# Kernel tuning notes

Measured on AMD Instinct MI355X. Metric: run time of the kernel, lower is better.

## Reference

```python
import jax, jax.numpy as jnp
import numpy as np

B, T, E, U, V = 4096, 80, 100, 64, 10000

def setup_inputs() -> dict:
    key = jax.random.key(0)
    ks = jax.random.split(key, 10)
    s = lambda *sh: 0.05
    return {
        "tokens": jax.random.randint(ks[0], (B, T), 0, V, dtype=jnp.int32),
        "emb": jax.random.normal(ks[1], (V, E), jnp.float32) * 0.05,
        "k0": jax.random.normal(ks[2], (E, 4 * U), jnp.float32) * 0.05,
        "r0": jax.random.normal(ks[3], (U, 4 * U), jnp.float32) * 0.05,
        "b0": jnp.zeros((4 * U,), jnp.float32),
        "k1": jax.random.normal(ks[4], (E, 4 * U), jnp.float32) * 0.05,
        "r1": jax.random.normal(ks[5], (U, 4 * U), jnp.float32) * 0.05,
        "b1": jnp.zeros((4 * U,), jnp.float32),
        "Wd": jax.random.normal(ks[6], (U, 1), jnp.float32) * 0.05,
        "bd": jnp.zeros((1,), jnp.float32),
    }

def _lstm_cell(h, c, xt, k, r, b):
    # keras LSTMCell gate order: i, f, g(cell candidate), o
    z = xt @ k + h @ r + b  # [B, 4U]
    i, f, g, o = jnp.split(z, 4, axis=-1)
    c_new = jax.nn.sigmoid(f) * c + jax.nn.sigmoid(i) * jnp.tanh(g)
    h_new = jax.nn.sigmoid(o) * jnp.tanh(c_new)
    return h_new, c_new

def reference(tokens, emb, k0, r0, b0, k1, r1, b1, Wd, bd):
    x = emb[tokens]                 # [B, T, E]
    xs = jnp.swapaxes(x, 0, 1)      # [T, B, E] for scan over time
    zeros = jnp.zeros((tokens.shape[0], U), x.dtype)
    init = (zeros, zeros, zeros, zeros)  # h0, c0, h1, c1

    def step(state, xt):
        h0, c0, h1, c1 = state
        h0, c0 = _lstm_cell(h0, c0, xt, k0, r0, b0)
        # NOTE: original feeds the raw embedded word (not out0) to cell 1
        h1, c1 = _lstm_cell(h1, c1, xt, k1, r1, b1)
        return (h0, c0, h1, c1), None

    (h0, c0, h1, c1), _ = jax.lax.scan(step, init, xs)
    logits = h1 @ Wd + bd           # [B, 1]
    return jax.nn.sigmoid(logits)
```

## Files before the change

kernel.cpp:

```cpp
#include <hip/hip_runtime.h>
#include <hip/hip_bf16.h>

#define B_  4096
#define T_  80
#define E_  100
#define U_  64
#define G_  256
#define V_  10000

#define S_H  72
#define AS   136

typedef __attribute__((ext_vector_type(8))) __bf16 bf16x8;
typedef __attribute__((ext_vector_type(4))) __bf16 bf16x4;
typedef __attribute__((ext_vector_type(4))) float  floatx4;

__device__ __forceinline__ float sigmoidf_(float x) {
    return __builtin_amdgcn_rcpf(1.f + __expf(-x));
}

__device__ __forceinline__ float tanhf_(float x) {
    return fmaf(-2.f, __builtin_amdgcn_rcpf(__expf(2.f * x) + 1.f), 1.f);
}

__device__ __forceinline__ void block_sync_lgkm() {
    asm volatile("s_waitcnt lgkmcnt(0)\n\ts_barrier" ::: "memory");
}

__global__ __launch_bounds__(256) void embk_kernel(const float* __restrict__ emb,
                                                   const float* __restrict__ k1,
                                                   const float* __restrict__ b1,
                                                   float* __restrict__ embk) {
    __shared__ __bf16 aLDS[64 * AS];

    const int tid  = threadIdx.x;
    const int lane = tid & 63;
    const int w    = tid >> 6;
    const int n    = lane & 15;
    const int kg   = lane >> 4;
    const int v0   = (blockIdx.x >> 1) * 64;
    const int n0   = (blockIdx.x & 1) * 128;
    const int nrows = min(64, V_ - v0);

    for (int i = tid; i < 64 * AS / 8; i += 256) {
        bf16x8 z;
#pragma unroll
        for (int jj = 0; jj < 8; ++jj) z[jj] = (__bf16)0.f;
        *(bf16x8*)(aLDS + i * 8) = z;
    }

    bf16x8 bfr[2][4];
#pragma unroll
    for (int ct = 0; ct < 2; ++ct)
#pragma unroll
        for (int kc = 0; kc < 4; ++kc) {
            bf16x8 s;
#pragma unroll
            for (int jj = 0; jj < 8; ++jj) {
                int k = kc * 32 + kg * 8 + jj;
                s[jj] = (k < E_) ? (__bf16)k1[k * G_ + n0 + w * 32 + ct * 16 + n]
                                 : (__bf16)0.f;
            }
            bfr[ct][kc] = s;
        }
    const float bv0 = b1[n0 + w * 32 + n];
    const float bv1 = b1[n0 + w * 32 + 16 + n];

    __syncthreads();

    for (int i = tid; i < nrows * 25; i += 256) {
        int r = i / 25, q = i - r * 25;
        float4 ev = *(const float4*)(emb + (long)(v0 + r) * E_ + q * 4);
        bf16x4 bv; bv[0] = (__bf16)ev.x; bv[1] = (__bf16)ev.y;
                   bv[2] = (__bf16)ev.z; bv[3] = (__bf16)ev.w;
        *(bf16x4*)(aLDS + r * AS + q * 4) = bv;
    }
    __syncthreads();

#pragma unroll
    for (int mt = 0; mt < 4; ++mt) {
        const __bf16* ab = aLDS + (mt * 16 + n) * AS + kg * 8;
        bf16x8 a0 = *(const bf16x8*)(ab + 0);
        bf16x8 a1 = *(const bf16x8*)(ab + 32);
        bf16x8 a2 = *(const bf16x8*)(ab + 64);
        bf16x8 a3 = *(const bf16x8*)(ab + 96);
#pragma unroll
        for (int ct = 0; ct < 2; ++ct) {
            float bv = ct ? bv1 : bv0;
            floatx4 acc = {bv, bv, bv, bv};
            acc = __builtin_amdgcn_mfma_f32_16x16x32_bf16(a0, bfr[ct][0], acc, 0, 0, 0);
            acc = __builtin_amdgcn_mfma_f32_16x16x32_bf16(a1, bfr[ct][1], acc, 0, 0, 0);
            acc = __builtin_amdgcn_mfma_f32_16x16x32_bf16(a2, bfr[ct][2], acc, 0, 0, 0);
            acc = __builtin_amdgcn_mfma_f32_16x16x32_bf16(a3, bfr[ct][3], acc, 0, 0, 0);
#pragma unroll
            for (int r = 0; r < 4; ++r) {
                int v = v0 + mt * 16 + kg * 4 + r;
                if (v < V_) embk[(long)v * G_ + n0 + w * 32 + ct * 16 + n] = acc[r];
            }
        }
    }
}

__global__ __launch_bounds__(256) void lstm_kernel(const int*   __restrict__ tokens,
                                                   const float* __restrict__ embk,
                                                   const float* __restrict__ r1,
                                                   const float* __restrict__ Wd,
                                                   const float* __restrict__ bd,
                                                   float* __restrict__ out) {
    __shared__ int    tokLDS[16 * T_];
    __shared__ __bf16 hbuf[2][16 * S_H];

    const int tid  = threadIdx.x;
    const int lane = tid & 63;
    const int w    = tid >> 6;
    const int n    = lane & 15;
    const int kg   = lane >> 4;
    const int bb   = blockIdx.x * 16;

    for (int i = tid; i < 16 * T_; i += 256) tokLDS[i] = tokens[bb * T_ + i];
    for (int i = tid; i < 2 * 16 * S_H; i += 256) (&hbuf[0][0])[i] = (__bf16)0.f;

    bf16x8 afr[4][2];
#pragma unroll
    for (int ct = 0; ct < 4; ++ct)
#pragma unroll
        for (int kc = 0; kc < 2; ++kc) {
            bf16x8 s;
#pragma unroll
            for (int jj = 0; jj < 8; ++jj)
                s[jj] = (__bf16)r1[(kc * 32 + kg * 8 + jj) * G_ + ct * 64 + w * 16 + n];
            afr[ct][kc] = s;
        }

    float c[4] = {0.f, 0.f, 0.f, 0.f};

    __syncthreads();

    floatx4 xkb[2][4];
#pragma unroll
    for (int s = 0; s < 2; ++s) {
        const float* base = embk + (long)tokLDS[n * T_ + s] * G_ + w * 16 + kg * 4;
#pragma unroll
        for (int ct = 0; ct < 4; ++ct)
            xkb[s][ct] = *(const floatx4*)(base + ct * 64);
    }

    auto step = [&](int t, int sel) {
        const __bf16* hb = hbuf[sel ^ 1];
        bf16x8 b0 = *(const bf16x8*)(hb + n * S_H + kg * 8);
        bf16x8 b1 = *(const bf16x8*)(hb + n * S_H + 32 + kg * 8);

        floatx4 acc[4];
#pragma unroll
        for (int ct = 0; ct < 4; ++ct) {
            floatx4 a = xkb[sel][ct];
            a = __builtin_amdgcn_mfma_f32_16x16x32_bf16(afr[ct][0], b0, a, 0, 0, 0);
            a = __builtin_amdgcn_mfma_f32_16x16x32_bf16(afr[ct][1], b1, a, 0, 0, 0);
            acc[ct] = a;
        }

        if (t + 2 < T_) {
            const float* base = embk + (long)tokLDS[n * T_ + t + 2] * G_ + w * 16 + kg * 4;
#pragma unroll
            for (int ct = 0; ct < 4; ++ct)
                xkb[sel][ct] = *(const floatx4*)(base + ct * 64);
        }

        bf16x4 hv;
#pragma unroll
        for (int r = 0; r < 4; ++r) {
            float zi = acc[0][r], zf = acc[1][r], zg = acc[2][r], zo = acc[3][r];
            float cn = fmaf(sigmoidf_(zf), c[r], sigmoidf_(zi) * tanhf_(zg));
            float hn = sigmoidf_(zo) * tanhf_(cn);
            c[r] = cn;
            hv[r] = (__bf16)hn;
        }
        *(bf16x4*)(&hbuf[sel][0] + n * S_H + w * 16 + kg * 4) = hv;

        block_sync_lgkm();
    };

    for (int t = 0; t < T_; t += 2) {
        step(t,     0);
        step(t + 1, 1);
    }

    if (tid < 16) {
        const __bf16* hb = hbuf[1] + tid * S_H;
        float s = bd[0];
#pragma unroll
        for (int u = 0; u < U_; ++u) s = fmaf((float)hb[u], Wd[u], s);
        out[bb + tid] = sigmoidf_(s);
    }
}

extern "C" void kernel_launch(void* const* d_in, const int* in_sizes, int n_in,
                              void* d_out, int out_size, void* d_ws, size_t ws_size,
                              hipStream_t stream) {
    const int*   tokens = (const int*)  d_in[0];
    const float* emb    = (const float*)d_in[1];
    const float* k1     = (const float*)d_in[5];
    const float* r1     = (const float*)d_in[6];
    const float* b1     = (const float*)d_in[7];
    const float* Wd     = (const float*)d_in[8];
    const float* bd     = (const float*)d_in[9];
    float*       out    = (float*)d_out;

    float* embk = (float*)d_ws;

    embk_kernel<<<((V_ + 63) / 64) * 2, 256, 0, stream>>>(emb, k1, b1, embk);
    lstm_kernel<<<B_ / 16, 256, 0, stream>>>(tokens, embk, r1, Wd, bd, out);
}
```

Before: 145.0 us.

## Fuse embedding-input projection into LSTM kernel with pipelined per-step MFMA

Drops the separate kernel that precomputed a V×4U table of embedding times k1 plus bias. The LSTM kernel now loads raw embedding rows for upcoming tokens and computes the input projection with extra MFMAs inside each step, using a two-stage prefetch (load for t+2, build for t+1). This removes one kernel launch and the 10 MB table write and read, at the cost of four times more MFMA work per step and higher register pressure from the k1 fragments. Launch bounds are set to one block per SM and the token LDS rows are padded to avoid bank conflicts.

```diff
diff --git a/kernel.cpp b/kernel.cpp
--- a/kernel.cpp
+++ b/kernel.cpp
@@ -9,7 +9,7 @@
 #define V_  10000
 
 #define S_H  72
-#define AS   136
+#define TS   81
 
 typedef __attribute__((ext_vector_type(8))) __bf16 bf16x8;
 typedef __attribute__((ext_vector_type(4))) __bf16 bf16x4;
@@ -27,87 +27,22 @@
     asm volatile("s_waitcnt lgkmcnt(0)\n\ts_barrier" ::: "memory");
 }
 
-__global__ __launch_bounds__(256) void embk_kernel(const float* __restrict__ emb,
-                                                   const float* __restrict__ k1,
-                                                   const float* __restrict__ b1,
-                                                   float* __restrict__ embk) {
-    __shared__ __bf16 aLDS[64 * AS];
-
-    const int tid  = threadIdx.x;
-    const int lane = tid & 63;
-    const int w    = tid >> 6;
-    const int n    = lane & 15;
-    const int kg   = lane >> 4;
-    const int v0   = (blockIdx.x >> 1) * 64;
-    const int n0   = (blockIdx.x & 1) * 128;
-    const int nrows = min(64, V_ - v0);
-
-    for (int i = tid; i < 64 * AS / 8; i += 256) {
-        bf16x8 z;
-#pragma unroll
-        for (int jj = 0; jj < 8; ++jj) z[jj] = (__bf16)0.f;
-        *(bf16x8*)(aLDS + i * 8) = z;
-    }
-
-    bf16x8 bfr[2][4];
-#pragma unroll
-    for (int ct = 0; ct < 2; ++ct)
-#pragma unroll
-        for (int kc = 0; kc < 4; ++kc) {
-            bf16x8 s;
-#pragma unroll
-            for (int jj = 0; jj < 8; ++jj) {
-                int k = kc * 32 + kg * 8 + jj;
-                s[jj] = (k < E_) ? (__bf16)k1[k * G_ + n0 + w * 32 + ct * 16 + n]
-                                 : (__bf16)0.f;
-            }
-            bfr[ct][kc] = s;
-        }
-    const float bv0 = b1[n0 + w * 32 + n];
-    const float bv1 = b1[n0 + w * 32 + 16 + n];
-
-    __syncthreads();
-
-    for (int i = tid; i < nrows * 25; i += 256) {
-        int r = i / 25, q = i - r * 25;
-        float4 ev = *(const float4*)(emb + (long)(v0 + r) * E_ + q * 4);
-        bf16x4 bv; bv[0] = (__bf16)ev.x; bv[1] = (__bf16)ev.y;
-                   bv[2] = (__bf16)ev.z; bv[3] = (__bf16)ev.w;
-        *(bf16x4*)(aLDS + r * AS + q * 4) = bv;
-    }
-    __syncthreads();
-
-#pragma unroll
-    for (int mt = 0; mt < 4; ++mt) {
-        const __bf16* ab = aLDS + (mt * 16 + n) * AS + kg * 8;
-        bf16x8 a0 = *(const bf16x8*)(ab + 0);
-        bf16x8 a1 = *(const bf16x8*)(ab + 32);
-        bf16x8 a2 = *(const bf16x8*)(ab + 64);
-        bf16x8 a3 = *(const bf16x8*)(ab + 96);
-#pragma unroll
-        for (int ct = 0; ct < 2; ++ct) {
-            float bv = ct ? bv1 : bv0;
-            floatx4 acc = {bv, bv, bv, bv};
-            acc = __builtin_amdgcn_mfma_f32_16x16x32_bf16(a0, bfr[ct][0], acc, 0, 0, 0);
-            acc = __builtin_amdgcn_mfma_f32_16x16x32_bf16(a1, bfr[ct][1], acc, 0, 0, 0);
-            acc = __builtin_amdgcn_mfma_f32_16x16x32_bf16(a2, bfr[ct][2], acc, 0, 0, 0);
-            acc = __builtin_amdgcn_mfma_f32_16x16x32_bf16(a3, bfr[ct][3], acc, 0, 0, 0);
-#pragma unroll
-            for (int r = 0; r < 4; ++r) {
-                int v = v0 + mt * 16 + kg * 4 + r;
-                if (v < V_) embk[(long)v * G_ + n0 + w * 32 + ct * 16 + n] = acc[r];
-            }
-        }
-    }
-}
-
-__global__ __launch_bounds__(256) void lstm_kernel(const int*   __restrict__ tokens,
-                                                   const float* __restrict__ embk,
-                                                   const float* __restrict__ r1,
-                                                   const float* __restrict__ Wd,
-                                                   const float* __restrict__ bd,
-                                                   float* __restrict__ out) {
-    __shared__ int    tokLDS[16 * T_];
+__device__ __forceinline__ bf16x8 cvt8(const float4& a, const float4& b) {
+    bf16x8 r;
+    r[0] = (__bf16)a.x; r[1] = (__bf16)a.y; r[2] = (__bf16)a.z; r[3] = (__bf16)a.w;
+    r[4] = (__bf16)b.x; r[5] = (__bf16)b.y; r[6] = (__bf16)b.z; r[7] = (__bf16)b.w;
+    return r;
+}
+
+__global__ __launch_bounds__(256, 1) void lstm_kernel(const int*   __restrict__ tokens,
+                                                      const float* __restrict__ emb,
+                                                      const float* __restrict__ k1,
+                                                      const float* __restrict__ r1,
+                                                      const float* __restrict__ b1,
+                                                      const float* __restrict__ Wd,
+                                                      const float* __restrict__ bd,
+                                                      float* __restrict__ out) {
+    __shared__ int    tokLDS[16 * TS];
     __shared__ __bf16 hbuf[2][16 * S_H];
 
     const int tid  = threadIdx.x;
@@ -117,7 +52,8 @@
     const int kg   = lane >> 4;
     const int bb   = blockIdx.x * 16;
 
-    for (int i = tid; i < 16 * T_; i += 256) tokLDS[i] = tokens[bb * T_ + i];
+    for (int i = tid; i < 16 * T_; i += 256)
+        tokLDS[(i / T_) * TS + (i % T_)] = tokens[bb * T_ + i];
     for (int i = tid; i < 2 * 16 * S_H; i += 256) (&hbuf[0][0])[i] = (__bf16)0.f;
 
     bf16x8 afr[4][2];
@@ -132,38 +68,92 @@
             afr[ct][kc] = s;
         }
 
+    bf16x8 kfr[4][4];
+#pragma unroll
+    for (int ct = 0; ct < 4; ++ct)
+#pragma unroll
+        for (int kc = 0; kc < 4; ++kc) {
+            bf16x8 s;
+#pragma unroll
+            for (int jj = 0; jj < 8; ++jj) {
+                int k = kc * 32 + kg * 8 + jj;
+                s[jj] = (k < E_) ? (__bf16)k1[k * G_ + ct * 64 + w * 16 + n]
+                                 : (__bf16)0.f;
+            }
+            kfr[ct][kc] = s;
+        }
+
+    floatx4 bias[4];
+#pragma unroll
+    for (int ct = 0; ct < 4; ++ct)
+#pragma unroll
+        for (int r = 0; r < 4; ++r)
+            bias[ct][r] = b1[ct * 64 + w * 16 + kg * 4 + r];
+
     float c[4] = {0.f, 0.f, 0.f, 0.f};
 
     __syncthreads();
 
-    floatx4 xkb[2][4];
-#pragma unroll
-    for (int s = 0; s < 2; ++s) {
-        const float* base = embk + (long)tokLDS[n * T_ + s] * G_ + w * 16 + kg * 4;
-#pragma unroll
-        for (int ct = 0; ct < 4; ++ct)
-            xkb[s][ct] = *(const floatx4*)(base + ct * 64);
-    }
-
-    auto step = [&](int t, int sel) {
-        const __bf16* hb = hbuf[sel ^ 1];
-        bf16x8 b0 = *(const bf16x8*)(hb + n * S_H + kg * 8);
-        bf16x8 b1 = *(const bf16x8*)(hb + n * S_H + 32 + kg * 8);
+    const int trow = n * TS;
+
+    auto ldstage = [&](int tk, float4* st) {
+        const float* base = emb + (long)tk * E_;
+#pragma unroll
+        for (int kc = 0; kc < 3; ++kc) {
+            st[kc * 2]     = *(const float4*)(base + kc * 32 + kg * 8);
+            st[kc * 2 + 1] = *(const float4*)(base + kc * 32 + kg * 8 + 4);
+        }
+        st[6] = *(const float4*)(base + 96);
+    };
+
+    auto xbuild = [&](const float4* st, floatx4* xo) {
+        bf16x8 x0 = cvt8(st[0], st[1]);
+        bf16x8 x1 = cvt8(st[2], st[3]);
+        bf16x8 x2 = cvt8(st[4], st[5]);
+        float4 e3 = st[6];
+        if (kg) { e3.x = 0.f; e3.y = 0.f; e3.z = 0.f; e3.w = 0.f; }
+        bf16x8 x3;
+        x3[0] = (__bf16)e3.x; x3[1] = (__bf16)e3.y;
+        x3[2] = (__bf16)e3.z; x3[3] = (__bf16)e3.w;
+        x3[4] = (__bf16)0.f;  x3[5] = (__bf16)0.f;
+        x3[6] = (__bf16)0.f;  x3[7] = (__bf16)0.f;
+#pragma unroll
+        for (int ct = 0; ct < 4; ++ct) {
+            floatx4 a = bias[ct];
+            a = __builtin_amdgcn_mfma_f32_16x16x32_bf16(kfr[ct][0], x0, a, 0, 0, 0);
+            a = __builtin_amdgcn_mfma_f32_16x16x32_bf16(kfr[ct][1], x1, a, 0, 0, 0);
+            a = __builtin_amdgcn_mfma_f32_16x16x32_bf16(kfr[ct][2], x2, a, 0, 0, 0);
+            a = __builtin_amdgcn_mfma_f32_16x16x32_bf16(kfr[ct][3], x3, a, 0, 0, 0);
+            xo[ct] = a;
+        }
+    };
+
+    float4  stA[7], stB[7];
+    floatx4 xaccA[4], xaccB[4];
+
+    ldstage(tokLDS[trow + 0], stA);
+    xbuild(stA, xaccA);
+    ldstage(tokLDS[trow + 1], stB);
+    int tkA = tokLDS[trow + 2];
+    int tkB = tokLDS[trow + 3];
+
+    auto step = [&](int t, const __bf16* hbR, __bf16* hbW,
+                    floatx4* xuse, floatx4* xbld,
+                    float4* stuse, float4* stbld, int& tkpf) {
+        bf16x8 b0  = *(const bf16x8*)(hbR + n * S_H + kg * 8);
+        bf16x8 b1v = *(const bf16x8*)(hbR + n * S_H + 32 + kg * 8);
+
+        ldstage(tkpf, stbld);
+        int tnext = t + 4; if (tnext > T_ - 1) tnext = T_ - 1;
+        tkpf = tokLDS[trow + tnext];
 
         floatx4 acc[4];
 #pragma unroll
         for (int ct = 0; ct < 4; ++ct) {
-            floatx4 a = xkb[sel][ct];
-            a = __builtin_amdgcn_mfma_f32_16x16x32_bf16(afr[ct][0], b0, a, 0, 0, 0);
-            a = __builtin_amdgcn_mfma_f32_16x16x32_bf16(afr[ct][1], b1, a, 0, 0, 0);
+            floatx4 a = xuse[ct];
+            a = __builtin_amdgcn_mfma_f32_16x16x32_bf16(afr[ct][0], b0,  a, 0, 0, 0);
+            a = __builtin_amdgcn_mfma_f32_16x16x32_bf16(afr[ct][1], b1v, a, 0, 0, 0);
             acc[ct] = a;
-        }
-
-        if (t + 2 < T_) {
-            const float* base = embk + (long)tokLDS[n * T_ + t + 2] * G_ + w * 16 + kg * 4;
-#pragma unroll
-            for (int ct = 0; ct < 4; ++ct)
-                xkb[sel][ct] = *(const floatx4*)(base + ct * 64);
         }
 
         bf16x4 hv;
@@ -175,14 +165,16 @@
             c[r] = cn;
             hv[r] = (__bf16)hn;
         }
-        *(bf16x4*)(&hbuf[sel][0] + n * S_H + w * 16 + kg * 4) = hv;
+        *(bf16x4*)(hbW + n * S_H + w * 16 + kg * 4) = hv;
+
+        xbuild(stuse, xbld);
 
         block_sync_lgkm();
     };
 
     for (int t = 0; t < T_; t += 2) {
-        step(t,     0);
-        step(t + 1, 1);
+        step(t,     hbuf[1], hbuf[0], xaccA, xaccB, stB, stA, tkA);
+        step(t + 1, hbuf[0], hbuf[1], xaccB, xaccA, stA, stB, tkB);
     }
 
     if (tid < 16) {
@@ -206,8 +198,5 @@
     const float* bd     = (const float*)d_in[9];
     float*       out    = (float*)d_out;
 
-    float* embk = (float*)d_ws;
-
-    embk_kernel<<<((V_ + 63) / 64) * 2, 256, 0, stream>>>(emb, k1, b1, embk);
-    lstm_kernel<<<B_ / 16, 256, 0, stream>>>(tokens, embk, r1, Wd, bd, out);
-}
+    lstm_kernel<<<B_ / 16, 256, 0, stream>>>(tokens, emb, k1, r1, b1, Wd, bd, out);
+}
```

New measurement: 154.2 us. 1.06x slower.

## Stage gathered embedding projections through LDS ring buffer with coalesced prefetch

Applied to the files above, without the earlier changes.

The LSTM kernel now gathers the per-token precomputed input projections with coalesced float4 loads (16 threads per row) into registers, writes them into a three-slot LDS ring, and reads them back in the MFMA accumulator layout. Before, each lane did scattered gathers straight into accumulator registers. The gather is issued three steps ahead to hide global latency behind the recurrence. The embk kernel also stages k1 through LDS with coalesced loads instead of strided scalar loads. The cost is extra LDS traffic and more shared memory per block, which may reduce occupancy.

```diff
diff --git a/kernel.cpp b/kernel.cpp
--- a/kernel.cpp
+++ b/kernel.cpp
@@ -10,6 +10,9 @@
 
 #define S_H  72
 #define AS   136
+#define KS2  132
+#define TS   81
+#define XS   260
 
 typedef __attribute__((ext_vector_type(8))) __bf16 bf16x8;
 typedef __attribute__((ext_vector_type(4))) __bf16 bf16x4;
@@ -32,6 +35,7 @@
                                                    const float* __restrict__ b1,
                                                    float* __restrict__ embk) {
     __shared__ __bf16 aLDS[64 * AS];
+    __shared__ __bf16 kLDS[128 * KS2];
 
     const int tid  = threadIdx.x;
     const int lane = tid & 63;
@@ -48,21 +52,9 @@
         for (int jj = 0; jj < 8; ++jj) z[jj] = (__bf16)0.f;
         *(bf16x8*)(aLDS + i * 8) = z;
     }
-
-    bf16x8 bfr[2][4];
-#pragma unroll
-    for (int ct = 0; ct < 2; ++ct)
-#pragma unroll
-        for (int kc = 0; kc < 4; ++kc) {
-            bf16x8 s;
-#pragma unroll
-            for (int jj = 0; jj < 8; ++jj) {
-                int k = kc * 32 + kg * 8 + jj;
-                s[jj] = (k < E_) ? (__bf16)k1[k * G_ + n0 + w * 32 + ct * 16 + n]
-                                 : (__bf16)0.f;
-            }
-            bfr[ct][kc] = s;
-        }
+    for (int i = tid; i < 28 * KS2; i += 256)
+        kLDS[100 * KS2 + i] = (__bf16)0.f;
+
     const float bv0 = b1[n0 + w * 32 + n];
     const float bv1 = b1[n0 + w * 32 + 16 + n];
 
@@ -75,7 +67,26 @@
                    bv[2] = (__bf16)ev.z; bv[3] = (__bf16)ev.w;
         *(bf16x4*)(aLDS + r * AS + q * 4) = bv;
     }
+    for (int i = tid; i < 100 * 32; i += 256) {
+        int k = i >> 5, cq = (i & 31) * 4;
+        float4 kv = *(const float4*)(k1 + (long)k * G_ + n0 + cq);
+        bf16x4 bv; bv[0] = (__bf16)kv.x; bv[1] = (__bf16)kv.y;
+                   bv[2] = (__bf16)kv.z; bv[3] = (__bf16)kv.w;
+        *(bf16x4*)(kLDS + k * KS2 + cq) = bv;
+    }
     __syncthreads();
+
+    bf16x8 bfr[2][4];
+#pragma unroll
+    for (int ct = 0; ct < 2; ++ct)
+#pragma unroll
+        for (int kc = 0; kc < 4; ++kc) {
+            bf16x8 s;
+#pragma unroll
+            for (int jj = 0; jj < 8; ++jj)
+                s[jj] = kLDS[(kc * 32 + kg * 8 + jj) * KS2 + w * 32 + ct * 16 + n];
+            bfr[ct][kc] = s;
+        }
 
 #pragma unroll
     for (int mt = 0; mt < 4; ++mt) {
@@ -107,8 +118,9 @@
                                                    const float* __restrict__ Wd,
                                                    const float* __restrict__ bd,
                                                    float* __restrict__ out) {
-    __shared__ int    tokLDS[16 * T_];
+    __shared__ int    tokLDS[16 * TS];
     __shared__ __bf16 hbuf[2][16 * S_H];
+    __shared__ float  xstage[3][16 * XS];
 
     const int tid  = threadIdx.x;
     const int lane = tid & 63;
@@ -116,8 +128,11 @@
     const int n    = lane & 15;
     const int kg   = lane >> 4;
     const int bb   = blockIdx.x * 16;
-
-    for (int i = tid; i < 16 * T_; i += 256) tokLDS[i] = tokens[bb * T_ + i];
+    const int prow = tid >> 4;
+    const int pp   = tid & 15;
+
+    for (int i = tid; i < 16 * T_; i += 256)
+        tokLDS[(i / T_) * TS + (i % T_)] = tokens[bb * T_ + i];
     for (int i = tid; i < 2 * 16 * S_H; i += 256) (&hbuf[0][0])[i] = (__bf16)0.f;
 
     bf16x8 afr[4][2];
@@ -136,34 +151,54 @@
 
     __syncthreads();
 
-    floatx4 xkb[2][4];
-#pragma unroll
-    for (int s = 0; s < 2; ++s) {
-        const float* base = embk + (long)tokLDS[n * T_ + s] * G_ + w * 16 + kg * 4;
-#pragma unroll
-        for (int ct = 0; ct < 4; ++ct)
-            xkb[s][ct] = *(const floatx4*)(base + ct * 64);
-    }
-
-    auto step = [&](int t, int sel) {
+    float4 pf[2][4];
+    {
+#pragma unroll
+        for (int s = 0; s < 2; ++s) {
+            const float* base = embk + (long)tokLDS[prow * TS + s] * G_ + pp * 4;
+            float* dst = xstage[s] + prow * XS + pp * 4;
+#pragma unroll
+            for (int j = 0; j < 4; ++j)
+                *(float4*)(dst + j * 64) = *(const float4*)(base + j * 64);
+        }
+        const float* base2 = embk + (long)tokLDS[prow * TS + 2] * G_ + pp * 4;
+#pragma unroll
+        for (int j = 0; j < 4; ++j)
+            pf[1][j] = *(const float4*)(base2 + j * 64);
+    }
+    block_sync_lgkm();
+
+    auto step = [&](int t, int sel, int rb, int wb) {
         const __bf16* hb = hbuf[sel ^ 1];
-        bf16x8 b0 = *(const bf16x8*)(hb + n * S_H + kg * 8);
-        bf16x8 b1 = *(const bf16x8*)(hb + n * S_H + 32 + kg * 8);
+        bf16x8 b0  = *(const bf16x8*)(hb + n * S_H + kg * 8);
+        bf16x8 b1v = *(const bf16x8*)(hb + n * S_H + 32 + kg * 8);
+        const float* xrow = xstage[rb] + n * XS + w * 16 + kg * 4;
+        floatx4 x0 = *(const floatx4*)(xrow + 0);
+        floatx4 x1 = *(const floatx4*)(xrow + 64);
+        floatx4 x2 = *(const floatx4*)(xrow + 128);
+        floatx4 x3 = *(const floatx4*)(xrow + 192);
+
+        {
+            float* dst = xstage[wb] + prow * XS + pp * 4;
+            *(float4*)(dst +   0) = pf[sel ^ 1][0];
+            *(float4*)(dst +  64) = pf[sel ^ 1][1];
+            *(float4*)(dst + 128) = pf[sel ^ 1][2];
+            *(float4*)(dst + 192) = pf[sel ^ 1][3];
+        }
+        {
+            int tt = t + 3; if (tt > T_ - 1) tt = T_ - 1;
+            const float* base = embk + (long)tokLDS[prow * TS + tt] * G_ + pp * 4;
+#pragma unroll
+            for (int j = 0; j < 4; ++j)
+                pf[sel][j] = *(const float4*)(base + j * 64);
+        }
 
         floatx4 acc[4];
+        acc[0] = x0; acc[1] = x1; acc[2] = x2; acc[3] = x3;
 #pragma unroll
         for (int ct = 0; ct < 4; ++ct) {
-            floatx4 a = xkb[sel][ct];
-            a = __builtin_amdgcn_mfma_f32_16x16x32_bf16(afr[ct][0], b0, a, 0, 0, 0);
-            a = __builtin_amdgcn_mfma_f32_16x16x32_bf16(afr[ct][1], b1, a, 0, 0, 0);
-            acc[ct] = a;
-        }
-
-        if (t + 2 < T_) {
-            const float* base = embk + (long)tokLDS[n * T_ + t + 2] * G_ + w * 16 + kg * 4;
-#pragma unroll
-            for (int ct = 0; ct < 4; ++ct)
-                xkb[sel][ct] = *(const floatx4*)(base + ct * 64);
+            acc[ct] = __builtin_amdgcn_mfma_f32_16x16x32_bf16(afr[ct][0], b0,  acc[ct], 0, 0, 0);
+            acc[ct] = __builtin_amdgcn_mfma_f32_16x16x32_bf16(afr[ct][1], b1v, acc[ct], 0, 0, 0);
         }
 
         bf16x4 hv;
@@ -180,10 +215,16 @@
         block_sync_lgkm();
     };
 
-    for (int t = 0; t < T_; t += 2) {
-        step(t,     0);
-        step(t + 1, 1);
-    }
+    for (int t = 0; t < 78; t += 6) {
+        step(t + 0, 0, 0, 2);
+        step(t + 1, 1, 1, 0);
+        step(t + 2, 0, 2, 1);
+        step(t + 3, 1, 0, 2);
+        step(t + 4, 0, 1, 0);
+        step(t + 5, 1, 2, 1);
+    }
+    step(78, 0, 0, 2);
+    step(79, 1, 1, 0);
 
     if (tid < 16) {
         const __bf16* hb = hbuf[1] + tid * S_H;
```

Result: slower. 176.7 us (+21.8%).

## Stage embedding-projection rows through LDS with async global_load_lds triple buffering

Applied to the files above, without the earlier changes.

The LSTM kernel now fetches the precomputed token-projection rows through a three-slot LDS staging buffer using global_load_lds, instead of per-lane register prefetch two steps ahead. Each step issues loads for step t+2 into the free slot, and the barrier waits on vmcnt(4) so only the older loads must complete. This takes the prefetch registers out of the recurrent loop and lets the DMA overlap compute, at the cost of more LDS and tight dependence on counter-based waits. The embk kernel also loads k1 coalesced into LDS before building its B fragments, replacing strided global reads.

```diff
diff --git a/kernel.cpp b/kernel.cpp
--- a/kernel.cpp
+++ b/kernel.cpp
@@ -1,5 +1,6 @@
 #include <hip/hip_runtime.h>
 #include <hip/hip_bf16.h>
+#include <stdint.h>
 
 #define B_  4096
 #define T_  80
@@ -10,6 +11,9 @@
 
 #define S_H  72
 #define AS   136
+#define KS2  132
+#define TS   81
+#define XS   260
 
 typedef __attribute__((ext_vector_type(8))) __bf16 bf16x8;
 typedef __attribute__((ext_vector_type(4))) __bf16 bf16x4;
@@ -23,8 +27,11 @@
     return fmaf(-2.f, __builtin_amdgcn_rcpf(__expf(2.f * x) + 1.f), 1.f);
 }
 
-__device__ __forceinline__ void block_sync_lgkm() {
-    asm volatile("s_waitcnt lgkmcnt(0)\n\ts_barrier" ::: "memory");
+__device__ __forceinline__ void gload16(const float* gsrc, const float* ldst) {
+    __builtin_amdgcn_global_load_lds(
+        (const __attribute__((address_space(1))) void*)(uintptr_t)gsrc,
+        (__attribute__((address_space(3))) void*)(uintptr_t)ldst,
+        16, 0, 0);
 }
 
 __global__ __launch_bounds__(256) void embk_kernel(const float* __restrict__ emb,
@@ -32,6 +39,7 @@
                                                    const float* __restrict__ b1,
                                                    float* __restrict__ embk) {
     __shared__ __bf16 aLDS[64 * AS];
+    __shared__ __bf16 kLDS[128 * KS2];
 
     const int tid  = threadIdx.x;
     const int lane = tid & 63;
@@ -48,21 +56,9 @@
         for (int jj = 0; jj < 8; ++jj) z[jj] = (__bf16)0.f;
         *(bf16x8*)(aLDS + i * 8) = z;
     }
-
-    bf16x8 bfr[2][4];
-#pragma unroll
-    for (int ct = 0; ct < 2; ++ct)
-#pragma unroll
-        for (int kc = 0; kc < 4; ++kc) {
-            bf16x8 s;
-#pragma unroll
-            for (int jj = 0; jj < 8; ++jj) {
-                int k = kc * 32 + kg * 8 + jj;
-                s[jj] = (k < E_) ? (__bf16)k1[k * G_ + n0 + w * 32 + ct * 16 + n]
-                                 : (__bf16)0.f;
-            }
-            bfr[ct][kc] = s;
-        }
+    for (int i = tid; i < 28 * KS2; i += 256)
+        kLDS[100 * KS2 + i] = (__bf16)0.f;
+
     const float bv0 = b1[n0 + w * 32 + n];
     const float bv1 = b1[n0 + w * 32 + 16 + n];
 
@@ -75,7 +71,26 @@
                    bv[2] = (__bf16)ev.z; bv[3] = (__bf16)ev.w;
         *(bf16x4*)(aLDS + r * AS + q * 4) = bv;
     }
+    for (int i = tid; i < 100 * 32; i += 256) {
+        int k = i >> 5, cq = (i & 31) * 4;
+        float4 kv = *(const float4*)(k1 + (long)k * G_ + n0 + cq);
+        bf16x4 bv; bv[0] = (__bf16)kv.x; bv[1] = (__bf16)kv.y;
+                   bv[2] = (__bf16)kv.z; bv[3] = (__bf16)kv.w;
+        *(bf16x4*)(kLDS + k * KS2 + cq) = bv;
+    }
     __syncthreads();
+
+    bf16x8 bfr[2][4];
+#pragma unroll
+    for (int ct = 0; ct < 2; ++ct)
+#pragma unroll
+        for (int kc = 0; kc < 4; ++kc) {
+            bf16x8 s;
+#pragma unroll
+            for (int jj = 0; jj < 8; ++jj)
+                s[jj] = kLDS[(kc * 32 + kg * 8 + jj) * KS2 + w * 32 + ct * 16 + n];
+            bfr[ct][kc] = s;
+        }
 
 #pragma unroll
     for (int mt = 0; mt < 4; ++mt) {
@@ -101,14 +116,63 @@
     }
 }
 
+template<int SEL, int RB, int WB>
+__device__ __forceinline__ void lstm_step(
+        int tt, int n, int kg, int w, int lane,
+        const int* __restrict__ tokLDS,
+        __bf16 (&hbuf)[2][16 * S_H],
+        float (&xstage)[3][16 * XS],
+        const bf16x8 (&afr)[4][2],
+        const float* __restrict__ embk,
+        float (&c)[4]) {
+    const __bf16* hb = &hbuf[SEL ^ 1][0];
+    bf16x8 hb0 = *(const bf16x8*)(hb + n * S_H + kg * 8);
+    bf16x8 hb1 = *(const bf16x8*)(hb + n * S_H + 32 + kg * 8);
+    const float* xrow = &xstage[RB][0] + n * XS + w * 16 + kg * 4;
+    floatx4 a0 = *(const floatx4*)(xrow + 0);
+    floatx4 a1 = *(const floatx4*)(xrow + 64);
+    floatx4 a2 = *(const floatx4*)(xrow + 128);
+    floatx4 a3 = *(const floatx4*)(xrow + 192);
+
+#pragma unroll
+    for (int j = 0; j < 4; ++j) {
+        int tok = tokLDS[(w * 4 + j) * TS + tt];
+        gload16(embk + (long)tok * G_ + (lane << 2),
+                &xstage[WB][0] + (w * 4 + j) * XS);
+    }
+
+    a0 = __builtin_amdgcn_mfma_f32_16x16x32_bf16(afr[0][0], hb0, a0, 0, 0, 0);
+    a0 = __builtin_amdgcn_mfma_f32_16x16x32_bf16(afr[0][1], hb1, a0, 0, 0, 0);
+    a1 = __builtin_amdgcn_mfma_f32_16x16x32_bf16(afr[1][0], hb0, a1, 0, 0, 0);
+    a1 = __builtin_amdgcn_mfma_f32_16x16x32_bf16(afr[1][1], hb1, a1, 0, 0, 0);
+    a2 = __builtin_amdgcn_mfma_f32_16x16x32_bf16(afr[2][0], hb0, a2, 0, 0, 0);
+    a2 = __builtin_amdgcn_mfma_f32_16x16x32_bf16(afr[2][1], hb1, a2, 0, 0, 0);
+    a3 = __builtin_amdgcn_mfma_f32_16x16x32_bf16(afr[3][0], hb0, a3, 0, 0, 0);
+    a3 = __builtin_amdgcn_mfma_f32_16x16x32_bf16(afr[3][1], hb1, a3, 0, 0, 0);
+
+    bf16x4 hv;
+#pragma unroll
+    for (int r = 0; r < 4; ++r) {
+        float zi = a0[r], zf = a1[r], zg = a2[r], zo = a3[r];
+        float cn = fmaf(sigmoidf_(zf), c[r], sigmoidf_(zi) * tanhf_(zg));
+        float hn = sigmoidf_(zo) * tanhf_(cn);
+        c[r] = cn;
+        hv[r] = (__bf16)hn;
+    }
+    *(bf16x4*)(&hbuf[SEL][0] + n * S_H + w * 16 + kg * 4) = hv;
+
+    asm volatile("s_waitcnt lgkmcnt(0) vmcnt(4)\n\ts_barrier" ::: "memory");
+}
+
 __global__ __launch_bounds__(256) void lstm_kernel(const int*   __restrict__ tokens,
                                                    const float* __restrict__ embk,
                                                    const float* __restrict__ r1,
                                                    const float* __restrict__ Wd,
                                                    const float* __restrict__ bd,
                                                    float* __restrict__ out) {
-    __shared__ int    tokLDS[16 * T_];
+    __shared__ int    tokLDS[16 * TS];
     __shared__ __bf16 hbuf[2][16 * S_H];
+    __shared__ float  xstage[3][16 * XS];
 
     const int tid  = threadIdx.x;
     const int lane = tid & 63;
@@ -117,7 +181,8 @@
     const int kg   = lane >> 4;
     const int bb   = blockIdx.x * 16;
 
-    for (int i = tid; i < 16 * T_; i += 256) tokLDS[i] = tokens[bb * T_ + i];
+    for (int i = tid; i < 16 * T_; i += 256)
+        tokLDS[(i / T_) * TS + (i % T_)] = tokens[bb * T_ + i];
     for (int i = tid; i < 2 * 16 * S_H; i += 256) (&hbuf[0][0])[i] = (__bf16)0.f;
 
     bf16x8 afr[4][2];
@@ -136,54 +201,28 @@
 
     __syncthreads();
 
-    floatx4 xkb[2][4];
-#pragma unroll
-    for (int s = 0; s < 2; ++s) {
-        const float* base = embk + (long)tokLDS[n * T_ + s] * G_ + w * 16 + kg * 4;
-#pragma unroll
-        for (int ct = 0; ct < 4; ++ct)
-            xkb[s][ct] = *(const floatx4*)(base + ct * 64);
-    }
-
-    auto step = [&](int t, int sel) {
-        const __bf16* hb = hbuf[sel ^ 1];
-        bf16x8 b0 = *(const bf16x8*)(hb + n * S_H + kg * 8);
-        bf16x8 b1 = *(const bf16x8*)(hb + n * S_H + 32 + kg * 8);
-
-        floatx4 acc[4];
-#pragma unroll
-        for (int ct = 0; ct < 4; ++ct) {
-            floatx4 a = xkb[sel][ct];
-            a = __builtin_amdgcn_mfma_f32_16x16x32_bf16(afr[ct][0], b0, a, 0, 0, 0);
-            a = __builtin_amdgcn_mfma_f32_16x16x32_bf16(afr[ct][1], b1, a, 0, 0, 0);
-            acc[ct] = a;
-        }
-
-        if (t + 2 < T_) {
-            const float* base = embk + (long)tokLDS[n * T_ + t + 2] * G_ + w * 16 + kg * 4;
-#pragma unroll
-            for (int ct = 0; ct < 4; ++ct)
-                xkb[sel][ct] = *(const floatx4*)(base + ct * 64);
-        }
-
-        bf16x4 hv;
-#pragma unroll
-        for (int r = 0; r < 4; ++r) {
-            float zi = acc[0][r], zf = acc[1][r], zg = acc[2][r], zo = acc[3][r];
-            float cn = fmaf(sigmoidf_(zf), c[r], sigmoidf_(zi) * tanhf_(zg));
-            float hn = sigmoidf_(zo) * tanhf_(cn);
-            c[r] = cn;
-            hv[r] = (__bf16)hn;
-        }
-        *(bf16x4*)(&hbuf[sel][0] + n * S_H + w * 16 + kg * 4) = hv;
-
-        block_sync_lgkm();
-    };
-
-    for (int t = 0; t < T_; t += 2) {
-        step(t,     0);
-        step(t + 1, 1);
-    }
+#pragma unroll
+    for (int s = 0; s < 2; ++s)
+#pragma unroll
+        for (int j = 0; j < 4; ++j) {
+            int tok = tokLDS[(w * 4 + j) * TS + s];
+            gload16(embk + (long)tok * G_ + (lane << 2),
+                    &xstage[s][0] + (w * 4 + j) * XS);
+        }
+    asm volatile("s_waitcnt lgkmcnt(0) vmcnt(4)\n\ts_barrier" ::: "memory");
+
+    for (int t = 0; t < 78; t += 6) {
+        lstm_step<0, 0, 2>(t + 2, n, kg, w, lane, tokLDS, hbuf, xstage, afr, embk, c);
+        lstm_step<1, 1, 0>(t + 3, n, kg, w, lane, tokLDS, hbuf, xstage, afr, embk, c);
+        lstm_step<0, 2, 1>(t + 4, n, kg, w, lane, tokLDS, hbuf, xstage, afr, embk, c);
+        lstm_step<1, 0, 2>(t + 5, n, kg, w, lane, tokLDS, hbuf, xstage, afr, embk, c);
+        lstm_step<0, 1, 0>(t + 6, n, kg, w, lane, tokLDS, hbuf, xstage, afr, embk, c);
+        lstm_step<1, 2, 1>(t + 7, n, kg, w, lane, tokLDS, hbuf, xstage, afr, embk, c);
+    }
+    lstm_step<0, 0, 2>(79, n, kg, w, lane, tokLDS, hbuf, xstage, afr, embk, c);
+    lstm_step<1, 1, 0>(79, n, kg, w, lane, tokLDS, hbuf, xstage, afr, embk, c);
+
+    asm volatile("s_waitcnt vmcnt(0)" ::: "memory");
 
     if (tid < 16) {
         const __bf16* hb = hbuf[1] + tid * S_H;
```

After: 135.5 us. 1.07x faster.
